# Kernel optimization log

Measured on AMD Instinct MI355X. Metric: run time of the kernel, lower is better.

Reference implementation:

```python
import jax, jax.numpy as jnp
import numpy as np

B = 128        # graphs per side
NPG = 512      # nodes per graph (equal-sized for jit)
N = B * NPG    # 65536 total nodes
E = 1048576    # edges per side
IN = 128       # input feature dim
H = 64         # hidden dim
BINS = 16      # histogram bins over [-1, 1]


def setup_inputs() -> dict:
    key = jax.random.key(0)
    ks = jax.random.split(key, 20)
    inp = {}
    inp["x1"] = jax.random.normal(ks[0], (N, IN), jnp.float32)
    inp["e1"] = jax.random.randint(ks[1], (2, E), 0, N)
    inp["b1"] = jnp.arange(N, dtype=jnp.int32) // NPG
    inp["x2"] = jax.random.normal(ks[2], (N, IN), jnp.float32)
    inp["e2"] = jax.random.randint(ks[3], (2, E), 0, N)
    inp["b2"] = jnp.arange(N, dtype=jnp.int32) // NPG
    def lin(k, fi, fo):
        s = 1.0 / np.sqrt(fi)
        return jax.random.uniform(k, (fi, fo), jnp.float32, -s, s)
    # GIN encoder (shared across both graph sides): conv1 MLP, conv2 MLP
    inp["enc_w1"] = lin(ks[4], IN, H); inp["enc_b1"] = jnp.zeros((H,), jnp.float32)
    inp["enc_w2"] = lin(ks[5], H, H);  inp["enc_b2"] = jnp.zeros((H,), jnp.float32)
    inp["enc_w3"] = lin(ks[6], H, H);  inp["enc_b3"] = jnp.zeros((H,), jnp.float32)
    inp["enc_w4"] = lin(ks[7], H, H);  inp["enc_b4"] = jnp.zeros((H,), jnp.float32)
    # final MLP: (2H + BINS + 3) -> H -> H//2 -> 1
    FIN = 2 * H + BINS + 3
    inp["mlp_w1"] = lin(ks[8], FIN, H);      inp["mlp_b1"] = jnp.zeros((H,), jnp.float32)
    inp["mlp_w2"] = lin(ks[9], H, H // 2);   inp["mlp_b2"] = jnp.zeros((H // 2,), jnp.float32)
    inp["mlp_w3"] = lin(ks[10], H // 2, 1);  inp["mlp_b3"] = jnp.zeros((1,), jnp.float32)
    return inp


def _gin_layer(x, src, dst, wa, ba, wb, bb):
    # GINConv (eps=0): mlp(x + sum_{j->i} x_j), then encoder-level ReLU
    agg = jax.ops.segment_sum(x[src], dst, num_segments=N)
    h = x + agg
    h = jnp.maximum(h @ wa + ba, 0.0) @ wb + bb
    return jnp.maximum(h, 0.0)


def _encode(x, e, enc_w1, enc_b1, enc_w2, enc_b2, enc_w3, enc_b3, enc_w4, enc_b4):
    src, dst = e[0], e[1]
    h = _gin_layer(x, src, dst, enc_w1, enc_b1, enc_w2, enc_b2)
    h = _gin_layer(h, src, dst, enc_w3, enc_b3, enc_w4, enc_b4)
    return h


def _hist_stats(h1, h2):
    # h1, h2: [N, H] node embeddings; equal-sized graphs -> [B, NPG, H]
    E1 = h1.reshape(B, NPG, H)
    E2 = h2.reshape(B, NPG, H)
    E1n = E1 / jnp.maximum(jnp.linalg.norm(E1, axis=-1, keepdims=True), 1e-12)
    E2n = E2 / jnp.maximum(jnp.linalg.norm(E2, axis=-1, keepdims=True), 1e-12)
    sim = jnp.einsum('bnd,bmd->bnm', E1n, E2n)          # [B, NPG, NPG]
    flat = sim.reshape(B, NPG * NPG)
    # histc over [-1, 1] with BINS bins (right-edge values go to last bin)
    idx = jnp.clip(jnp.floor((flat + 1.0) * (BINS / 2.0)), 0, BINS - 1).astype(jnp.int32)
    seg = (jnp.arange(B, dtype=jnp.int32)[:, None] * BINS + idx).reshape(-1)
    hist = jax.ops.segment_sum(jnp.ones((B * NPG * NPG,), jnp.float32), seg,
                               num_segments=B * BINS).reshape(B, BINS)
    hist = hist / jnp.maximum(hist.sum(axis=1, keepdims=True), 1.0)
    stats = jnp.stack([flat.mean(axis=1), flat.max(axis=1), flat.std(axis=1)], axis=1)
    return jnp.concatenate([hist, stats], axis=1)        # [B, BINS+3]


def reference(x1, e1, b1, x2, e2, b2,
              enc_w1, enc_b1, enc_w2, enc_b2, enc_w3, enc_b3, enc_w4, enc_b4,
              mlp_w1, mlp_b1, mlp_w2, mlp_b2, mlp_w3, mlp_b3):
    h1 = _encode(x1, e1, enc_w1, enc_b1, enc_w2, enc_b2, enc_w3, enc_b3, enc_w4, enc_b4)
    h2 = _encode(x2, e2, enc_w1, enc_b1, enc_w2, enc_b2, enc_w3, enc_b3, enc_w4, enc_b4)
    # global_mean_pool: equal-sized contiguous graphs -> reshape mean
    g1 = h1.reshape(B, NPG, H).mean(axis=1)
    g2 = h2.reshape(B, NPG, H).mean(axis=1)
    sim_feats = _hist_stats(h1, h2)
    f = jnp.concatenate([g1, g2, sim_feats], axis=1)     # [B, 2H+BINS+3]
    f = jnp.maximum(f @ mlp_w1 + mlp_b1, 0.0)            # dropout = identity (eval)
    f = jnp.maximum(f @ mlp_w2 + mlp_b2, 0.0)
    out = (f @ mlp_w3 + mlp_b3)[:, 0]                    # [B]
    return out
```

## Files before the change

### kernel.cpp

```cpp
#include <hip/hip_runtime.h>
#include <hip/hip_bf16.h>
#include <hip/hip_fp16.h>

namespace {

constexpr int N    = 65536;
constexpr int E    = 1048576;
constexpr int N2   = 2 * N;
constexpr int B    = 128;
constexpr int NPG  = 512;
constexpr int IN   = 128;
constexpr int H    = 64;
constexpr int BINS = 16;
constexpr int FIN  = 2 * H + BINS + 3;
constexpr int NBUCKET = 512;
constexpr int NSLICE  = 512;
constexpr int SLICE_E = 4096;

typedef _Float16 f16x8 __attribute__((ext_vector_type(8)));
typedef float f32x16 __attribute__((ext_vector_type(16)));

union FragU { f16x8 v; unsigned int u[4]; };

__device__ __forceinline__ unsigned packh(float a, float b) {
  typedef __fp16 fp16x2 __attribute__((ext_vector_type(2)));
  union { fp16x2 h; unsigned u; } t;
  t.h = __builtin_amdgcn_cvt_pkrtz(a, b);
  return t.u;
}

__device__ __forceinline__ f16x8 ldf16x8(const __half* p) {
  return *(const f16x8*)(const void*)p;
}

__device__ __forceinline__ void xw_tile(int nodebase, int lane, const float* __restrict__ x1,
                                        const float* __restrict__ x2, const float* __restrict__ W,
                                        __half* __restrict__ y) {
  const float* xp = (nodebase < N) ? (x1 + (size_t)nodebase * IN)
                                   : (x2 + (size_t)(nodebase - N) * IN);
  int r = lane & 31;
  int kh = lane >> 5;
  const float* xrow = xp + (size_t)r * IN + kh * 8;
  f32x16 acc0, acc1;
#pragma unroll
  for (int i = 0; i < 16; ++i) { acc0[i] = 0.f; acc1[i] = 0.f; }
#pragma unroll
  for (int kk = 0; kk < 8; ++kk) {
    float4 a0 = *(const float4*)(xrow + kk * 16);
    float4 a1 = *(const float4*)(xrow + kk * 16 + 4);
    f16x8 af;
    af[0] = (_Float16)a0.x; af[1] = (_Float16)a0.y; af[2] = (_Float16)a0.z; af[3] = (_Float16)a0.w;
    af[4] = (_Float16)a1.x; af[5] = (_Float16)a1.y; af[6] = (_Float16)a1.z; af[7] = (_Float16)a1.w;
    const float* wbase = W + (size_t)(kk * 16 + kh * 8) * H + r;
    f16x8 b0, b1;
#pragma unroll
    for (int j = 0; j < 8; ++j) {
      b0[j] = (_Float16)wbase[j * H];
      b1[j] = (_Float16)wbase[j * H + 32];
    }
    acc0 = __builtin_amdgcn_mfma_f32_32x32x16_f16(af, b0, acc0, 0, 0, 0);
    acc1 = __builtin_amdgcn_mfma_f32_32x32x16_f16(af, b1, acc1, 0, 0, 0);
  }
#pragma unroll
  for (int reg = 0; reg < 16; ++reg) {
    int row = (reg & 3) + 8 * (reg >> 2) + 4 * kh;
    y[(size_t)(nodebase + row) * H + r]      = __float2half(acc0[reg]);
    y[(size_t)(nodebase + row) * H + r + 32] = __float2half(acc1[reg]);
  }
}

__global__ __launch_bounds__(256) void k_hist(const int* __restrict__ dst1, const int* __restrict__ dst2,
                                              int* __restrict__ bcnt,
                                              const float* __restrict__ Wa, const float* __restrict__ Wb,
                                              const float* __restrict__ Wc, __half* __restrict__ WaT,
                                              __half* __restrict__ WbT, __half* __restrict__ WcT) {
  __shared__ int hist[NBUCKET];
  int b = blockIdx.x, tid = threadIdx.x;
  if (b < NSLICE) {
    hist[tid] = 0;
    hist[tid + 256] = 0;
    __syncthreads();
    const int* d = (b < 256) ? dst1 : dst2;
    int ebase = (b & 255) * SLICE_E;
    int boff = (b < 256) ? 0 : 256;
    for (int i = tid; i < SLICE_E; i += 256) atomicAdd(&hist[boff + (d[ebase + i] >> 8)], 1);
    __syncthreads();
    for (int k = tid; k < NBUCKET; k += 256) bcnt[b * NBUCKET + k] = hist[k];
  } else {
    int i = (b - NSLICE) * 256 + tid;
    int k = i >> 6, h = i & 63;
    WaT[h * 64 + k] = __float2half(Wa[k * 64 + h]);
    WbT[h * 64 + k] = __float2half(Wb[k * 64 + h]);
    WcT[h * 64 + k] = __float2half(Wc[k * 64 + h]);
  }
}

__global__ __launch_bounds__(256) void k_scan_xw(const int* __restrict__ bcnt, int* __restrict__ boffs,
                                                 int* __restrict__ tot,
                                                 const float* __restrict__ x1, const float* __restrict__ x2,
                                                 const float* __restrict__ W, __half* __restrict__ y) {
  __shared__ int s[NSLICE];
  int b = blockIdx.x, t = threadIdx.x;
  if (b < NBUCKET) {
    int v0 = bcnt[t * NBUCKET + b], v1 = bcnt[(t + 256) * NBUCKET + b];
    s[t] = v0;
    s[t + 256] = v1;
    __syncthreads();
    for (int d = 1; d < NSLICE; d <<= 1) {
      int a0 = (t >= d) ? s[t - d] : 0;
      int a1 = (t + 256 >= d) ? s[t + 256 - d] : 0;
      __syncthreads();
      s[t] += a0;
      s[t + 256] += a1;
      __syncthreads();
    }
    boffs[b * NSLICE + t] = s[t] - v0;
    boffs[b * NSLICE + t + 256] = s[t + 256] - v1;
    if (t == 255) tot[b] = s[NSLICE - 1];
  } else {
    int wv = t >> 6, lane = t & 63;
    int nodebase = ((b - NBUCKET) * 4 + wv) * 32;
    xw_tile(nodebase, lane, x1, x2, W, y);
  }
}

__global__ __launch_bounds__(256) void k_p5_xw(const int* __restrict__ src1, const int* __restrict__ dst1,
                                               const int* __restrict__ src2, const int* __restrict__ dst2,
                                               const int* __restrict__ boffs, const int* __restrict__ tot,
                                               int* __restrict__ ebuf,
                                               const float* __restrict__ x1, const float* __restrict__ x2,
                                               const float* __restrict__ W, __half* __restrict__ y) {
  __shared__ int stot[NBUCKET];
  __shared__ int sofs[NBUCKET];
  __shared__ int cur[NBUCKET];
  int b = blockIdx.x, tid = threadIdx.x;
  if (b < NSLICE) {
    int v0 = tot[tid], v1 = tot[tid + 256];
    stot[tid] = v0;
    stot[tid + 256] = v1;
    __syncthreads();
    for (int d = 1; d < NBUCKET; d <<= 1) {
      int a0 = (tid >= d) ? stot[tid - d] : 0;
      int a1 = (tid + 256 >= d) ? stot[tid + 256 - d] : 0;
      __syncthreads();
      stot[tid] += a0;
      stot[tid + 256] += a1;
      __syncthreads();
    }
    sofs[tid]       = stot[tid] - v0 + boffs[tid * NSLICE + b];
    sofs[tid + 256] = stot[tid + 256] - v1 + boffs[(tid + 256) * NSLICE + b];
    cur[tid] = 0;
    cur[tid + 256] = 0;
    __syncthreads();
    const int* sr = (b < 256) ? src1 : src2;
    const int* d  = (b < 256) ? dst1 : dst2;
    int ebase = (b & 255) * SLICE_E;
    int off = (b < 256) ? 0 : N;
    int boff2 = (b < 256) ? 0 : 256;
    for (int i = tid; i < SLICE_E; i += 256) {
      int dd = d[ebase + i];
      int sv = off + sr[ebase + i];
      int bucket = boff2 + (dd >> 8);
      int r = atomicAdd(&cur[bucket], 1);
      ebuf[sofs[bucket] + r] = ((dd & 255) << 17) | sv;
    }
  } else {
    int wv = tid >> 6, lane = tid & 63;
    int nodebase = N + ((b - NSLICE) * 4 + wv) * 32;
    xw_tile(nodebase, lane, x1, x2, W, y);
  }
}

__global__ __launch_bounds__(256) void k_p6(const int* __restrict__ ebuf, const int* __restrict__ tot,
                                            int* __restrict__ rowptr, int* __restrict__ col) {
  __shared__ int stot[NBUCKET];
  __shared__ int c256[256];
  __shared__ int lofs[256];
  int b = blockIdx.x, t = threadIdx.x;
  {
    int v0 = tot[t], v1 = tot[t + 256];
    stot[t] = v0;
    stot[t + 256] = v1;
    __syncthreads();
    for (int d = 1; d < NBUCKET; d <<= 1) {
      int a0 = (t >= d) ? stot[t - d] : 0;
      int a1 = (t + 256 >= d) ? stot[t + 256 - d] : 0;
      __syncthreads();
      stot[t] += a0;
      stot[t + 256] += a1;
      __syncthreads();
    }
  }
  int e0 = (b == 0) ? 0 : stot[b - 1];
  int e1 = stot[b];
  c256[t] = 0;
  __syncthreads();
  for (int i = e0 + t; i < e1; i += 256) atomicAdd(&c256[(ebuf[i] >> 17) & 255], 1);
  __syncthreads();
  int v = c256[t];
  lofs[t] = v;
  __syncthreads();
  for (int d = 1; d < 256; d <<= 1) {
    int a = (t >= d) ? lofs[t - d] : 0;
    __syncthreads();
    lofs[t] += a;
    __syncthreads();
  }
  int excl = lofs[t] - v;
  rowptr[b * 256 + t] = e0 + excl;
  if (b == 0 && t == 0) rowptr[N2] = 2 * E;
  c256[t] = 0;
  lofs[t] = excl;
  __syncthreads();
  for (int i = e0 + t; i < e1; i += 256) {
    int pk = ebuf[i];
    int dl = (pk >> 17) & 255;
    int r = atomicAdd(&c256[dl], 1);
    col[e0 + lofs[dl] + r] = pk & 0x1FFFF;
  }
}


__global__ __launch_bounds__(256) void k_gather(const __half* __restrict__ in, const int* __restrict__ rowptr,
                                                const int* __restrict__ col, const float* __restrict__ bias,
                                                __half* __restrict__ outb) {
  int tid = threadIdx.x;
  int lane32 = tid & 31;
  int n = blockIdx.x * 8 + (tid >> 5);
  const __half2* in2 = (const __half2*)in;
  __half2* out2 = (__half2*)outb;
  float2 bias2 = ((const float2*)bias)[lane32];
  int p0 = rowptr[n], p1 = rowptr[n + 1];
  int deg = p1 - p0;
  int pc = (p1 - 1 > p0) ? p1 - 1 : p0;
  int cidx = p0 + lane32;
  int c0 = col[cidx < pc ? cidx : pc];
  __half2 self = in2[(size_t)n * 32 + lane32];
  float ax = __half2float(self.x) + bias2.x;
  float ay = __half2float(self.y) + bias2.y;
  float cx = 0.f, cy = 0.f;
  if (deg > 0) {
    __half2 vl;
    {
      __half2 v[16];
#pragma unroll
      for (int i = 0; i < 16; ++i) {
        int c = __shfl(c0, i, 32);
        v[i] = in2[(size_t)c * 32 + lane32];
      }
#pragma unroll
      for (int i = 0; i < 16; i += 4) {
        __half2 w0 = __hadd2(v[i], v[i + 1]);
        __half2 w1 = __hadd2(v[i + 2], v[i + 3]);
        ax += __half2float(w0.x);
        ay += __half2float(w0.y);
        cx += __half2float(w1.x);
        cy += __half2float(w1.y);
      }
      vl = v[15];
    }
    if (deg > 16) {
      __half2 v[16];
#pragma unroll
      for (int i = 0; i < 16; ++i) {
        int c = __shfl(c0, i + 16, 32);
        v[i] = in2[(size_t)c * 32 + lane32];
      }
#pragma unroll
      for (int i = 0; i < 16; i += 4) {
        __half2 w0 = __hadd2(v[i], v[i + 1]);
        __half2 w1 = __hadd2(v[i + 2], v[i + 3]);
        ax += __half2float(w0.x);
        ay += __half2float(w0.y);
        cx += __half2float(w1.x);
        cy += __half2float(w1.y);
      }
      vl = v[15];
    }
    if (deg > 32) {
      for (int p = p0 + 32; p < p1; ++p) {
        int c = col[p];
        __half2 v = in2[(size_t)c * 32 + lane32];
        ax += __half2float(v.x);
        ay += __half2float(v.y);
      }
    }
    int cov = (deg > 16) ? 32 : 16;
    int dup = cov - (deg < cov ? deg : cov);
    float fd = (float)dup;
    ax -= fd * __half2float(vl.x);
    ay -= fd * __half2float(vl.y);
  }
  __half2 o;
  o.x = __float2half(fmaxf(ax + cx, 0.f));
  o.y = __float2half(fmaxf(ay + cy, 0.f));
  out2[(size_t)n * 32 + lane32] = o;
}

__global__ __launch_bounds__(256) void k_mid(const __half* __restrict__ in, const __half* __restrict__ WaT,
                                             const float* __restrict__ ba, const __half* __restrict__ WbT,
                                             __half* __restrict__ outb) {
  int tid = threadIdx.x, wv = tid >> 6, lane = tid & 63;
  int nodebase = (blockIdx.x * 4 + wv) * 32;
  int r = lane & 31, kh = lane >> 5;
  f32x16 acc0, acc1;
#pragma unroll
  for (int i = 0; i < 16; ++i) { acc0[i] = 0.f; acc1[i] = 0.f; }
  const __half* brow = in + (size_t)(nodebase + r) * H + kh * 8;
#pragma unroll
  for (int kk = 0; kk < 4; ++kk) {
    f16x8 bf = ldf16x8(brow + kk * 16);
    f16x8 a0 = ldf16x8(WaT + (size_t)r * H + kk * 16 + kh * 8);
    f16x8 a1 = ldf16x8(WaT + (size_t)(r + 32) * H + kk * 16 + kh * 8);
    acc0 = __builtin_amdgcn_mfma_f32_32x32x16_f16(a0, bf, acc0, 0, 0, 0);
    acc1 = __builtin_amdgcn_mfma_f32_32x32x16_f16(a1, bf, acc1, 0, 0, 0);
  }
  float bav = ba[lane];
  unsigned p0[8], p1[8];
#pragma unroll
  for (int g2 = 0; g2 < 8; ++g2) {
    int regA = 2 * g2, regB = 2 * g2 + 1;
    int rowA = (regA & 3) + 8 * (regA >> 2) + 4 * kh;
    int rowB = (regB & 3) + 8 * (regB >> 2) + 4 * kh;
    float tA0 = fmaxf(acc0[regA] + __shfl(bav, rowA, 64), 0.f);
    float tB0 = fmaxf(acc0[regB] + __shfl(bav, rowB, 64), 0.f);
    float tA1 = fmaxf(acc1[regA] + __shfl(bav, rowA + 32, 64), 0.f);
    float tB1 = fmaxf(acc1[regB] + __shfl(bav, rowB + 32, 64), 0.f);
    p0[g2] = packh(tA0, tB0);
    p1[g2] = packh(tA1, tB1);
  }
  unsigned q0[8], q1[8];
#pragma unroll
  for (int i = 0; i < 8; ++i) {
    q0[i] = (unsigned)__shfl_xor((int)p0[i], 32, 64);
    q1[i] = (unsigned)__shfl_xor((int)p1[i], 32, 64);
  }
  bool hi = (kh != 0);
  f32x16 o0, o1;
#pragma unroll
  for (int i = 0; i < 16; ++i) { o0[i] = 0.f; o1[i] = 0.f; }
#pragma unroll
  for (int kk = 0; kk < 4; ++kk) {
    const unsigned* P = (kk < 2) ? p0 : p1;
    const unsigned* Q = (kk < 2) ? q0 : q1;
    int s = kk & 1;
    FragU f;
    f.u[0] = hi ? Q[4 * s + 2] : P[4 * s + 0];
    f.u[1] = hi ? Q[4 * s + 3] : P[4 * s + 1];
    f.u[2] = hi ? P[4 * s + 2] : Q[4 * s + 0];
    f.u[3] = hi ? P[4 * s + 3] : Q[4 * s + 1];
    f16x8 b0 = ldf16x8(WbT + (size_t)r * H + kk * 16 + kh * 8);
    f16x8 b1 = ldf16x8(WbT + (size_t)(r + 32) * H + kk * 16 + kh * 8);
    o0 = __builtin_amdgcn_mfma_f32_32x32x16_f16(f.v, b0, o0, 0, 0, 0);
    o1 = __builtin_amdgcn_mfma_f32_32x32x16_f16(f.v, b1, o1, 0, 0, 0);
  }
#pragma unroll
  for (int reg = 0; reg < 16; ++reg) {
    int row = (reg & 3) + 8 * (reg >> 2) + 4 * kh;
    outb[(size_t)(nodebase + row) * H + r]      = __float2half(o0[reg]);
    outb[(size_t)(nodebase + row) * H + r + 32] = __float2half(o1[reg]);
  }
}

__global__ __launch_bounds__(256) void k_last(const __half* __restrict__ in, const __half* __restrict__ WcT,
                                              const float* __restrict__ b4, __half* __restrict__ outn,
                                              float* __restrict__ pg) {
  int tid = threadIdx.x, wv = tid >> 6, lane = tid & 63;
  int tile = blockIdx.x * 4 + wv;
  int nodebase = tile * 32;
  int r = lane & 31, kh = lane >> 5;
  f32x16 acc0, acc1;
#pragma unroll
  for (int i = 0; i < 16; ++i) { acc0[i] = 0.f; acc1[i] = 0.f; }
  const __half* arow = in + (size_t)(nodebase + r) * H + kh * 8;
#pragma unroll
  for (int kk = 0; kk < 4; ++kk) {
    f16x8 af = ldf16x8(arow + kk * 16);
    f16x8 b0 = ldf16x8(WcT + (size_t)r * H + kk * 16 + kh * 8);
    f16x8 b1 = ldf16x8(WcT + (size_t)(r + 32) * H + kk * 16 + kh * 8);
    acc0 = __builtin_amdgcn_mfma_f32_32x32x16_f16(af, b0, acc0, 0, 0, 0);
    acc1 = __builtin_amdgcn_mfma_f32_32x32x16_f16(af, b1, acc1, 0, 0, 0);
  }
  float bA = b4[r], bB = b4[r + 32];
  float psum0 = 0.f, psum1 = 0.f;
#pragma unroll
  for (int reg = 0; reg < 16; ++reg) {
    int row = (reg & 3) + 8 * (reg >> 2) + 4 * kh;
    float h0 = fmaxf(acc0[reg] + bA, 0.f);
    float h1 = fmaxf(acc1[reg] + bB, 0.f);
    psum0 += h0;
    psum1 += h1;
    float ss = h0 * h0 + h1 * h1;
#pragma unroll
    for (int d = 1; d < 32; d <<= 1) ss += __shfl_xor(ss, d, 64);
    float inv = 1.f / fmaxf(sqrtf(ss), 1e-12f);
    outn[(size_t)(nodebase + row) * H + r]      = __float2half(h0 * inv);
    outn[(size_t)(nodebase + row) * H + r + 32] = __float2half(h1 * inv);
  }
  psum0 += __shfl_xor(psum0, 32, 64);
  psum1 += __shfl_xor(psum1, 32, 64);
  if (kh == 0) {
    pg[tile * 64 + r]      = psum0;
    pg[tile * 64 + r + 32] = psum1;
  }
}

__global__ __launch_bounds__(256) void k_sim(const __half* __restrict__ Hn, float* __restrict__ psum,
                                             float* __restrict__ psumsq, float* __restrict__ pmax,
                                             int* __restrict__ phist) {
  __shared__ int shist[64 * 17];
  __shared__ float sfin[4][4];
  int tid = threadIdx.x, lane = tid & 63, wv = tid >> 6;
  int g = blockIdx.x >> 3, rt = blockIdx.x & 7;
  for (int i = tid; i < 64 * 17; i += 256) shist[i] = 0;
  __syncthreads();

  int rtile = wv & 1;
  int cgrp  = wv >> 1;
  int arow = lane & 31;
  int koff = (lane >> 5) * 8;

  const __half* H1 = Hn + ((size_t)g * NPG + rt * 64 + rtile * 32 + arow) * H + koff;
  f16x8 afrag[4];
#pragma unroll
  for (int kk = 0; kk < 4; ++kk) afrag[kk] = ldf16x8(H1 + kk * 16);

  const __half* H2g = Hn + ((size_t)N + (size_t)g * NPG + arow) * H + koff;
  float lmax = -2.f, lsum = 0.f, lsumsq = 0.f;
  int rep = lane * 17;
#pragma unroll 1
  for (int t = 0; t < 8; ++t) {
    int ct = cgrp * 8 + t;
    const __half* B0 = H2g + (size_t)(ct * 32) * H;
    f32x16 acc;
#pragma unroll
    for (int r = 0; r < 16; ++r) acc[r] = 0.f;
#pragma unroll
    for (int kk = 0; kk < 4; ++kk) {
      f16x8 bfrag = ldf16x8(B0 + kk * 16);
      acc = __builtin_amdgcn_mfma_f32_32x32x16_f16(afrag[kk], bfrag, acc, 0, 0, 0);
    }
#pragma unroll
    for (int r = 0; r < 16; ++r) {
      float v = acc[r];
      lmax = fmaxf(lmax, v);
      lsum += v;
      lsumsq = fmaf(v, v, lsumsq);
      int bin = (int)((v + 1.f) * 8.f);
      bin = bin < 0 ? 0 : (bin > BINS - 1 ? BINS - 1 : bin);
      atomicAdd(&shist[rep + bin], 1);
    }
  }
#pragma unroll
  for (int d = 1; d < 64; d <<= 1) {
    lsum += __shfl_xor(lsum, d, 64);
    lsumsq += __shfl_xor(lsumsq, d, 64);
    lmax = fmaxf(lmax, __shfl_xor(lmax, d, 64));
  }
  if (lane == 0) {
    sfin[wv][0] = lsum;
    sfin[wv][1] = lsumsq;
    sfin[wv][2] = lmax;
  }
  __syncthreads();
  if (tid == 0) {
    psum[blockIdx.x] = sfin[0][0] + sfin[1][0] + sfin[2][0] + sfin[3][0];
    psumsq[blockIdx.x] = sfin[0][1] + sfin[1][1] + sfin[2][1] + sfin[3][1];
    pmax[blockIdx.x] = fmaxf(fmaxf(sfin[0][2], sfin[1][2]), fmaxf(sfin[2][2], sfin[3][2]));
  }
  if (tid < BINS) {
    int tot = 0;
    for (int r = 0; r < 64; ++r) tot += shist[r * 17 + tid];
    phist[blockIdx.x * BINS + tid] = tot;
  }
}

__global__ __launch_bounds__(64) void k_final(const float* __restrict__ pg1, const float* __restrict__ pg2,
                                              const float* __restrict__ psum, const float* __restrict__ psumsq,
                                              const float* __restrict__ pmax, const int* __restrict__ phist,
                                              const float* __restrict__ w1, const float* __restrict__ b1,
                                              const float* __restrict__ w2, const float* __restrict__ b2,
                                              const float* __restrict__ w3, const float* __restrict__ b3,
                                              float* __restrict__ out) {
  __shared__ float f[FIN + 1];
  __shared__ float t1[64];
  __shared__ float t2[32];
  int g = blockIdx.x, t = threadIdx.x;
  {
    float s1v = 0.f, s2v = 0.f;
#pragma unroll
    for (int r = 0; r < 16; ++r) {
      s1v += pg1[(g * 16 + r) * 64 + t];
      s2v += pg2[(g * 16 + r) * 64 + t];
    }
    f[t]      = s1v * (1.f / NPG);
    f[64 + t] = s2v * (1.f / NPG);
  }
  if (t < BINS) {
    int tot = 0;
#pragma unroll
    for (int r = 0; r < 8; ++r) tot += phist[(g * 8 + r) * BINS + t];
    f[2 * H + t] = (float)tot * (1.f / 262144.f);
  }
  if (t == 0) {
    float s = 0.f, ss = 0.f, mx = -2.f;
#pragma unroll
    for (int r = 0; r < 8; ++r) {
      s += psum[g * 8 + r];
      ss += psumsq[g * 8 + r];
      mx = fmaxf(mx, pmax[g * 8 + r]);
    }
    const float inv = 1.f / 262144.f;
    float mean = s * inv;
    float var = fmaxf(ss * inv - mean * mean, 0.f);
    f[144] = mean;
    f[145] = mx;
    f[146] = sqrtf(var);
  }
  __syncthreads();
  float acc = b1[t];
  for (int k = 0; k < FIN; ++k) acc = fmaf(f[k], w1[k * 64 + t], acc);
  t1[t] = fmaxf(acc, 0.f);
  __syncthreads();
  if (t < 32) {
    float a2 = b2[t];
#pragma unroll 8
    for (int k = 0; k < 64; ++k) a2 = fmaf(t1[k], w2[k * 32 + t], a2);
    t2[t] = fmaxf(a2, 0.f);
  }
  __syncthreads();
  if (t == 0) {
    float a3 = b3[0];
#pragma unroll
    for (int k = 0; k < 32; ++k) a3 = fmaf(t2[k], w3[k], a3);
    out[g] = a3;
  }
}

}

extern "C" void kernel_launch(void* const* d_in, const int* in_sizes, int n_in, void* d_out, int out_size,
                              void* d_ws, size_t ws_size, hipStream_t stream) {
  const float* x1 = (const float*)d_in[0];
  const int* e1 = (const int*)d_in[1];
  const float* x2 = (const float*)d_in[3];
  const int* e2 = (const int*)d_in[4];
  const float* enc_w1 = (const float*)d_in[6];
  const float* enc_b1 = (const float*)d_in[7];
  const float* enc_w2 = (const float*)d_in[8];
  const float* enc_b2 = (const float*)d_in[9];
  const float* enc_w3 = (const float*)d_in[10];
  const float* enc_b3 = (const float*)d_in[11];
  const float* enc_w4 = (const float*)d_in[12];
  const float* enc_b4 = (const float*)d_in[13];
  const float* mw1 = (const float*)d_in[14];
  const float* mb1 = (const float*)d_in[15];
  const float* mw2 = (const float*)d_in[16];
  const float* mb2 = (const float*)d_in[17];
  const float* mw3 = (const float*)d_in[18];
  const float* mb3 = (const float*)d_in[19];
  float* out = (float*)d_out;

  char* wsc = (char*)d_ws;
  size_t off = 0;
  auto alloc = [&](size_t bytes) -> void* {
    void* p = wsc + off;
    off += (bytes + 255) & ~(size_t)255;
    return p;
  };
  __half* Hn = (__half*)alloc((size_t)N2 * H * 2);
  __half* yH = (__half*)alloc((size_t)N2 * H * 2);
  __half* tH = (__half*)alloc((size_t)N2 * H * 2);
  __half* zH = (__half*)alloc((size_t)N2 * H * 2);
  __half* t2H = (__half*)alloc((size_t)N2 * H * 2);
  int* rowptr = (int*)alloc((size_t)(N2 + 1) * 4);
  int* colidx = (int*)alloc((size_t)2 * E * 4);
  int* bcnt = (int*)alloc((size_t)NSLICE * NBUCKET * 4);
  int* boffs = (int*)alloc((size_t)NBUCKET * NSLICE * 4);
  int* tot = (int*)alloc((size_t)NBUCKET * 4);
  float* pg = (float*)alloc((size_t)(N2 / 32) * 64 * 4);
  float* psum = (float*)alloc(1024 * 4);
  float* psumsq = (float*)alloc(1024 * 4);
  float* pmaxa = (float*)alloc(1024 * 4);
  int* phist = (int*)alloc((size_t)1024 * BINS * 4);
  __half* WaT = (__half*)alloc(4096 * 2);
  __half* WbT = (__half*)alloc(4096 * 2);
  __half* WcT = (__half*)alloc(4096 * 2);
  (void)ws_size;
  (void)in_sizes;
  (void)n_in;
  (void)out_size;

  const int* src1 = e1;
  const int* dst1 = e1 + E;
  const int* src2 = e2;
  const int* dst2 = e2 + E;
  int* ebuf = (int*)tH;

  k_hist<<<NSLICE + 16, 256, 0, stream>>>(dst1, dst2, bcnt, enc_w2, enc_w3, enc_w4, WaT, WbT, WcT);
  k_scan_xw<<<NBUCKET + 512, 256, 0, stream>>>(bcnt, boffs, tot, x1, x2, enc_w1, yH);
  k_p5_xw<<<NSLICE + 512, 256, 0, stream>>>(src1, dst1, src2, dst2, boffs, tot, ebuf, x1, x2, enc_w1, yH);
  k_p6<<<NBUCKET, 256, 0, stream>>>(ebuf, tot, rowptr, colidx);

  k_gather<<<N2 / 8, 256, 0, stream>>>(yH, rowptr, colidx, enc_b1, tH);
  k_mid<<<N2 / 128, 256, 0, stream>>>(tH, WaT, enc_b2, WbT, zH);
  k_gather<<<N2 / 8, 256, 0, stream>>>(zH, rowptr, colidx, enc_b3, t2H);
  k_last<<<N2 / 128, 256, 0, stream>>>(t2H, WcT, enc_b4, Hn, pg);

  k_sim<<<B * 8, 256, 0, stream>>>(Hn, psum, psumsq, pmaxa, phist);
  k_final<<<B, 64, 0, stream>>>(pg, pg + (size_t)2048 * 64, psum, psumsq, pmaxa, phist, mw1, mb1, mw2, mb2,
                                mw3, mb3, out);
}
```

Measured before the change: 185.8 us.

## Stage bucketed edge scatter through shared memory for coalesced global writes

The edge-bucketing pass now records each edge's bucket and rank in registers, scans the per-slice bucket counts, and reorders the slice's edges in shared memory by bucket before writing them out. Each thread then writes consecutive sorted entries, so writes into the same bucket's destination range land next to each other instead of scattering randomly. This adds 32KB of LDS per block, an extra block-wide scan and several barriers, which may lower occupancy for the fused xw blocks sharing this kernel.

```diff
diff --git a/kernel.cpp b/kernel.cpp
--- a/kernel.cpp
+++ b/kernel.cpp
@@ -132,7 +132,10 @@
                                                const float* __restrict__ W, __half* __restrict__ y) {
   __shared__ int stot[NBUCKET];
   __shared__ int sofs[NBUCKET];
-  __shared__ int cur[NBUCKET];
+  __shared__ int cnt[NBUCKET];
+  __shared__ int lofs[NBUCKET];
+  __shared__ int sortedv[SLICE_E];
+  __shared__ int sorteda[SLICE_E];
   int b = blockIdx.x, tid = threadIdx.x;
   if (b < NSLICE) {
     int v0 = tot[tid], v1 = tot[tid + 256];
@@ -149,20 +152,54 @@
     }
     sofs[tid]       = stot[tid] - v0 + boffs[tid * NSLICE + b];
     sofs[tid + 256] = stot[tid + 256] - v1 + boffs[(tid + 256) * NSLICE + b];
-    cur[tid] = 0;
-    cur[tid + 256] = 0;
+    cnt[tid] = 0;
+    cnt[tid + 256] = 0;
     __syncthreads();
     const int* sr = (b < 256) ? src1 : src2;
     const int* d  = (b < 256) ? dst1 : dst2;
     int ebase = (b & 255) * SLICE_E;
     int off = (b < 256) ? 0 : N;
     int boff2 = (b < 256) ? 0 : 256;
-    for (int i = tid; i < SLICE_E; i += 256) {
-      int dd = d[ebase + i];
-      int sv = off + sr[ebase + i];
+    int rb[16], vals[16];
+#pragma unroll
+    for (int i = 0; i < 16; ++i) {
+      int e = ebase + tid + 256 * i;
+      int dd = d[e];
+      int sv = off + sr[e];
       int bucket = boff2 + (dd >> 8);
-      int r = atomicAdd(&cur[bucket], 1);
-      ebuf[sofs[bucket] + r] = ((dd & 255) << 17) | sv;
+      int r = atomicAdd(&cnt[bucket], 1);
+      rb[i] = (bucket << 12) | r;
+      vals[i] = ((dd & 255) << 17) | sv;
+    }
+    __syncthreads();
+    int c0 = cnt[tid], c1 = cnt[tid + 256];
+    stot[tid] = c0;
+    stot[tid + 256] = c1;
+    __syncthreads();
+    for (int d2 = 1; d2 < NBUCKET; d2 <<= 1) {
+      int a0 = (tid >= d2) ? stot[tid - d2] : 0;
+      int a1 = (tid + 256 >= d2) ? stot[tid + 256 - d2] : 0;
+      __syncthreads();
+      stot[tid] += a0;
+      stot[tid + 256] += a1;
+      __syncthreads();
+    }
+    lofs[tid] = stot[tid] - c0;
+    lofs[tid + 256] = stot[tid + 256] - c1;
+    __syncthreads();
+#pragma unroll
+    for (int i = 0; i < 16; ++i) {
+      int bucket = rb[i] >> 12;
+      int r = rb[i] & 4095;
+      int lp = lofs[bucket] + r;
+      sortedv[lp] = vals[i];
+      sorteda[lp] = sofs[bucket] + r;
+    }
+    __syncthreads();
+#pragma unroll
+    for (int i = 0; i < 16; ++i) {
+      int idx = tid + 256 * i;
+      ebuf[sorteda[idx]] = sortedv[idx];
     }
   } else {
     int wv = tid >> 6, lane = tid & 63;
```

New measurement: 179.9 us. -3.2%, faster.
